# Kernel tuning notes

Hardware: AMD Instinct MI355X
Metric: run time of the kernel (lower is better)

The kernel has to match this reference:

```python
import jax, jax.numpy as jnp
import numpy as np

NUM_HEADS = 4
LN_EPS = 1e-5


def _gcn_layer(src, dst, feats, skip_w, skip_b, msg_w, msg_b):
    # DGL GCNLayer: symmetric degree norm (from src rows), copy_u+sum aggregation,
    # msg linear + affine skip. No activation is applied in the original forward.
    n = feats.shape[0]
    deg = jax.ops.segment_sum(jnp.ones(src.shape, feats.dtype), src, num_segments=n)
    dinv = jnp.where(deg > 0, deg ** -0.5, jnp.zeros_like(deg))
    h = feats * dinv[:, None]                                  # [N, D]
    agg = jax.ops.segment_sum(h[src], dst, num_segments=n)     # scatter-sum over edges
    rst = agg * dinv[:, None]
    return rst @ msg_w.T + msg_b + feats @ skip_w.T + skip_b


def _layernorm(x, g, b):
    mu = jnp.mean(x, axis=-1, keepdims=True)
    var = jnp.mean((x - mu) ** 2, axis=-1, keepdims=True)
    return (x - mu) * jax.lax.rsqrt(var + LN_EPS) * g + b


def _cross_attention(x, seq, in_proj_w, in_proj_b, out_proj_w, out_proj_b, ln_g, ln_b):
    # Unbatched torch nn.MultiheadAttention(query=x [N,D], key=value=seq [S,D]).
    n, d = x.shape
    hd = d // NUM_HEADS
    wq, wk, wv = in_proj_w[:d], in_proj_w[d:2 * d], in_proj_w[2 * d:]
    bq, bk, bv = in_proj_b[:d], in_proj_b[d:2 * d], in_proj_b[2 * d:]
    q = (x @ wq.T + bq).reshape(n, NUM_HEADS, hd)
    k = (seq @ wk.T + bk).reshape(-1, NUM_HEADS, hd)
    v = (seq @ wv.T + bv).reshape(-1, NUM_HEADS, hd)
    scores = jnp.einsum('nhd,shd->hns', q, k) / jnp.sqrt(jnp.asarray(hd, x.dtype))
    attn = jax.nn.softmax(scores, axis=-1)
    o = jnp.einsum('hns,shd->nhd', attn, v).reshape(n, d)
    o = o @ out_proj_w.T + out_proj_b
    # dropout is identity in eval mode; residual + layernorm (num_cross_att == 1 path)
    return _layernorm(o + x, ln_g, ln_b)


def reference(x, seq_embeddings, src, dst, edge_label_index,
              skip_w0, skip_b0, msg_w0, msg_b0,
              skip_w1, skip_b1, msg_w1, msg_b1,
              in_proj_w, in_proj_b, out_proj_w, out_proj_b, ln_g, ln_b,
              weight1, weight2):
    x = _gcn_layer(src, dst, x, skip_w0, skip_b0, msg_w0, msg_b0)
    x = _gcn_layer(src, dst, x, skip_w1, skip_b1, msg_w1, msg_b1)
    x = _cross_attention(x, seq_embeddings, in_proj_w, in_proj_b,
                         out_proj_w, out_proj_b, ln_g, ln_b)
    # F.normalize: row-wise L2
    x = x / jnp.maximum(jnp.linalg.norm(x, axis=-1, keepdims=True), 1e-12)
    node_embedding = x
    p = jax.nn.relu(x @ weight1.T)                # dropout identity (eval)
    p = jax.nn.sigmoid(p @ weight2.T)[:, 0]       # [N]
    # dot edge decoding over last dim of size 1 -> elementwise product
    pred = p[edge_label_index[0]] * p[edge_label_index[1]]
    return pred, node_embedding


def setup_inputs() -> dict:
    key = jax.random.key(0)
    ks = jax.random.split(key, 20)
    N, E, S, D, K = 8192, 524288, 2048, 128, 100000
    s = 1.0 / np.sqrt(D)  # xavier-ish scale for weight matrices
    inp = {
        'x': jax.random.normal(ks[0], (N, D), jnp.float32),
        'seq_embeddings': jax.random.normal(ks[1], (S, D), jnp.float32),
        'src': jax.random.randint(ks[2], (E,), 0, N, jnp.int32),
        'dst': jax.random.randint(ks[3], (E,), 0, N, jnp.int32),
        'edge_label_index': jax.random.randint(ks[4], (2, K), 0, N, jnp.int32),
        'skip_w0': jax.random.normal(ks[5], (D, D), jnp.float32) * s,
        'skip_b0': jnp.zeros((D,), jnp.float32),
        'msg_w0': jax.random.normal(ks[6], (D, D), jnp.float32) * s,
        'msg_b0': jnp.zeros((D,), jnp.float32),
        'skip_w1': jax.random.normal(ks[7], (D, D), jnp.float32) * s,
        'skip_b1': jnp.zeros((D,), jnp.float32),
        'msg_w1': jax.random.normal(ks[8], (D, D), jnp.float32) * s,
        'msg_b1': jnp.zeros((D,), jnp.float32),
        'in_proj_w': jax.random.normal(ks[9], (3 * D, D), jnp.float32) * s,
        'in_proj_b': jnp.zeros((3 * D,), jnp.float32),
        'out_proj_w': jax.random.normal(ks[10], (D, D), jnp.float32) * s,
        'out_proj_b': jnp.zeros((D,), jnp.float32),
        'ln_g': jnp.ones((D,), jnp.float32),
        'ln_b': jnp.zeros((D,), jnp.float32),
        'weight1': jax.random.normal(ks[11], (D, D), jnp.float32) * s,
        'weight2': jax.random.normal(ks[12], (1, D), jnp.float32) * s,
    }
    return inp
```

## Files before the change

kernel.cpp:

```cpp
#include <hip/hip_runtime.h>
#include <math.h>

#define D 128
#define HB 128
#define FA_PS 88

typedef short bf16x4 __attribute__((ext_vector_type(4)));
typedef short bf16x8 __attribute__((ext_vector_type(8)));
typedef float f32x4 __attribute__((ext_vector_type(4)));

__device__ __forceinline__ float4 ld4(const float* p) { return *(const float4*)p; }

__device__ __forceinline__ short f2bf_r(float f) {
  return (short)((__float_as_uint(f) + 0x8000u) >> 16);
}
__device__ __forceinline__ float bf2f(short s) {
  return __uint_as_float(((unsigned)(unsigned short)s) << 16);
}
__device__ __forceinline__ unsigned pack_bf2(float a, float b) {
  unsigned ua = __float_as_uint(a) + 0x8000u;
  unsigned ub = __float_as_uint(b) + 0x8000u;
  return __builtin_amdgcn_perm(ub, ua, 0x07060302);
}

struct WSrc { const float* p[9]; };
__global__ __launch_bounds__(256) void prep0_kernel(WSrc ws, short* __restrict__ Wbf,
                                                    const float* __restrict__ x,
                                                    short* __restrict__ xbf) {
  int b = blockIdx.x, t = threadIdx.x;
  if (b < 144) {
    int m = b >> 4, blk = b & 15;
    int i = (blk * 256 + t) * 4;
    float4 v = ld4(ws.p[m] + i);
    bf16x4 o = {f2bf_r(v.x), f2bf_r(v.y), f2bf_r(v.z), f2bf_r(v.w)};
    *(bf16x4*)&Wbf[m * 16384 + i] = o;
  } else {
    int i = ((b - 144) * 256 + t) * 4;
    float4 v = ld4(x + i);
    bf16x4 o = {f2bf_r(v.x), f2bf_r(v.y), f2bf_r(v.z), f2bf_r(v.w)};
    *(bf16x4*)&xbf[i] = o;
  }
}

__global__ __launch_bounds__(256) void hist_kernel(
    const int* __restrict__ src, const int* __restrict__ dst,
    int* __restrict__ histd, int* __restrict__ hists, int E) {
  __shared__ int hd[8192];
  __shared__ int hs[8192];
  int t = threadIdx.x;
  for (int i = t; i < 8192; i += 256) { hd[i] = 0; hs[i] = 0; }
  __syncthreads();
  int per = E / HB;
  int b0 = blockIdx.x * per;
  for (int j = 0; j < per; j += 256) {
    int i = b0 + j + t;
    atomicAdd(&hd[dst[i]], 1);
    atomicAdd(&hs[src[i]], 1);
  }
  __syncthreads();
  for (int i = t; i < 8192; i += 256) {
    histd[blockIdx.x * 8192 + i] = hd[i];
    hists[blockIdx.x * 8192 + i] = hs[i];
  }
}

__global__ __launch_bounds__(256) void colsum_kernel(
    const int* __restrict__ histd, const int* __restrict__ hists,
    int* __restrict__ deg, float* __restrict__ dinv) {
  int v = blockIdx.x * 256 + threadIdx.x;
  int sd = 0, ss = 0;
  for (int b = 0; b < HB; ++b) { sd += histd[b * 8192 + v]; ss += hists[b * 8192 + v]; }
  deg[v] = sd;
  dinv[v] = ss > 0 ? rsqrtf((float)ss) : 0.f;
}

__global__ __launch_bounds__(1024) void scan8k_kernel(
    const int* __restrict__ deg, int* __restrict__ row_ptr, int N) {
  __shared__ int wtot[16];
  int t = threadIdx.x;
  int lane = t & 63, wv = t >> 6;
  int v0 = t * 8;
  int x[8]; int s = 0;
#pragma unroll
  for (int j = 0; j < 8; ++j) { x[j] = s; s += deg[v0 + j]; }
  int incl = s;
  for (int off = 1; off < 64; off <<= 1) {
    int y = __shfl_up(incl, off);
    if (lane >= off) incl += y;
  }
  if (lane == 63) wtot[wv] = incl;
  __syncthreads();
  if (t == 0) { int run = 0; for (int i = 0; i < 16; ++i) { int v = wtot[i]; wtot[i] = run; run += v; } }
  __syncthreads();
  int base = wtot[wv] + (incl - s);
#pragma unroll
  for (int j = 0; j < 8; ++j) row_ptr[v0 + j] = base + x[j];
  if (t == 1023) row_ptr[N] = base + s;
}

__global__ __launch_bounds__(256) void basegen_kernel(
    const int* __restrict__ histd, const int* __restrict__ row_ptr,
    int* __restrict__ base_arr) {
  int v = blockIdx.x * 256 + threadIdx.x;
  int run = row_ptr[v];
  for (int b = 0; b < HB; ++b) { base_arr[b * 8192 + v] = run; run += histd[b * 8192 + v]; }
}

__global__ __launch_bounds__(256) void scatter2_kernel(
    const int* __restrict__ src, const int* __restrict__ dst,
    const int* __restrict__ base_arr, int* __restrict__ csr_src, int E) {
  __shared__ int lh[8192];
  int t = threadIdx.x;
  for (int i = t; i < 8192; i += 256) lh[i] = 0;
  __syncthreads();
  int per = E / HB;
  int b0 = blockIdx.x * per;
  const int* __restrict__ bb = &base_arr[blockIdx.x * 8192];
  for (int j = 0; j < per; j += 256) {
    int i = b0 + j + t;
    int v = dst[i];
    int r = atomicAdd(&lh[v], 1);
    csr_src[bb[v] + r] = src[i];
  }
}

__global__ __launch_bounds__(128) void agg_kernel(
    const short* __restrict__ fbf, const float* __restrict__ dinv,
    const int* __restrict__ row_ptr, const int* __restrict__ csr_src,
    short* __restrict__ outbf) {
  __shared__ int idx[128];
  __shared__ float dv[128];
  __shared__ float red[8][128];
  int n = blockIdx.x, t = threadIdx.x;
  int grp = t >> 4, l16 = t & 15;
  int beg = row_ptr[n], end = row_ptr[n + 1];
  float a0[8] = {}, a1[8] = {};
  for (int c = beg; c < end; c += 128) {
    int j = c + t;
    if (j < end) { int s = csr_src[j]; idx[t] = s; dv[t] = dinv[s]; }
    __syncthreads();
    int cnt = min(128, end - c);
    int e = grp;
    for (; e + 8 < cnt; e += 16) {
      bf16x8 w0 = *(const bf16x8*)&fbf[(size_t)idx[e] * D + l16 * 8];
      bf16x8 w1 = *(const bf16x8*)&fbf[(size_t)idx[e + 8] * D + l16 * 8];
      float wt0 = dv[e], wt1 = dv[e + 8];
#pragma unroll
      for (int k = 0; k < 8; ++k) {
        a0[k] += bf2f(w0[k]) * wt0;
        a1[k] += bf2f(w1[k]) * wt1;
      }
    }
    for (; e < cnt; e += 8) {
      bf16x8 w0 = *(const bf16x8*)&fbf[(size_t)idx[e] * D + l16 * 8];
      float wt0 = dv[e];
#pragma unroll
      for (int k = 0; k < 8; ++k) a0[k] += bf2f(w0[k]) * wt0;
    }
    __syncthreads();
  }
#pragma unroll
  for (int k = 0; k < 8; ++k) a0[k] += a1[k];
  *(float4*)&red[grp][l16 * 8] = *(float4*)&a0[0];
  *(float4*)&red[grp][l16 * 8 + 4] = *(float4*)&a0[4];
  __syncthreads();
  if (t < 32) {
    int d0 = t * 4;
    float o[4] = {};
#pragma unroll
    for (int g = 0; g < 8; ++g) {
      o[0] += red[g][d0]; o[1] += red[g][d0 + 1];
      o[2] += red[g][d0 + 2]; o[3] += red[g][d0 + 3];
    }
    float w = dinv[n];
    bf16x4 ov = {f2bf_r(o[0] * w), f2bf_r(o[1] * w), f2bf_r(o[2] * w), f2bf_r(o[3] * w)};
    *(bf16x4*)&outbf[(size_t)n * D + d0] = ov;
  }
}

__device__ __forceinline__ void mfma_accum(const short* As, const short* __restrict__ W,
                                           int rt, int ch, int quad, int r16, f32x4* acc) {
#pragma unroll
  for (int ks = 0; ks < 4; ++ks) {
    bf16x8 af = *(bf16x8*)&As[(rt * 16 + r16) * 136 + ks * 32 + quad * 8];
#pragma unroll
    for (int nt = 0; nt < 4; ++nt) {
      bf16x8 bw = *(const bf16x8*)&W[(size_t)(ch * 64 + nt * 16 + r16) * D + ks * 32 + quad * 8];
      acc[nt] = __builtin_amdgcn_mfma_f32_16x16x32_bf16(af, bw, acc[nt], 0, 0, 0);
    }
  }
}

__device__ __forceinline__ void stage_A_f32(const float* __restrict__ A, int m0, short* As) {
  int row = threadIdx.x >> 3, seg = threadIdx.x & 7;
  const float* ap = &A[(size_t)(m0 + row) * D + seg * 16];
  float4 v0 = ld4(ap), v1 = ld4(ap + 4), v2 = ld4(ap + 8), v3 = ld4(ap + 12);
  bf16x8 w0 = {f2bf_r(v0.x), f2bf_r(v0.y), f2bf_r(v0.z), f2bf_r(v0.w),
               f2bf_r(v1.x), f2bf_r(v1.y), f2bf_r(v1.z), f2bf_r(v1.w)};
  bf16x8 w1 = {f2bf_r(v2.x), f2bf_r(v2.y), f2bf_r(v2.z), f2bf_r(v2.w),
               f2bf_r(v3.x), f2bf_r(v3.y), f2bf_r(v3.z), f2bf_r(v3.w)};
  *(bf16x8*)&As[row * 136 + seg * 16] = w0;
  *(bf16x8*)&As[row * 136 + seg * 16 + 8] = w1;
}

__device__ __forceinline__ void stage_A_bf16(const short* __restrict__ A, int m0, short* As) {
  int row = threadIdx.x >> 3, seg = threadIdx.x & 7;
  const short* ap = &A[(size_t)(m0 + row) * D + seg * 16];
  bf16x8 a0 = *(const bf16x8*)ap;
  bf16x8 a1 = *(const bf16x8*)(ap + 8);
  *(bf16x8*)&As[row * 136 + seg * 16] = a0;
  *(bf16x8*)&As[row * 136 + seg * 16 + 8] = a1;
}

__global__ __launch_bounds__(256) void gemm_gcn_kernel(
    const short* __restrict__ A1, const short* __restrict__ W1, const float* __restrict__ b1,
    const short* __restrict__ A2, const short* __restrict__ W2, const float* __restrict__ b2,
    short* __restrict__ Cbf, float* __restrict__ Cf) {
  __shared__ short As[32 * 136];
  const int t = threadIdx.x;
  const int m0 = blockIdx.x * 32;
  const int w = t >> 6, lane = t & 63, quad = lane >> 4, r16 = lane & 15;
  const int rt = w & 1, ch = w >> 1;
  f32x4 acc[4];
  f32x4 zz = {0.f, 0.f, 0.f, 0.f};
  acc[0] = zz; acc[1] = zz; acc[2] = zz; acc[3] = zz;
  stage_A_bf16(A1, m0, As);
  __syncthreads();
  mfma_accum(As, W1, rt, ch, quad, r16, acc);
  __syncthreads();
  stage_A_bf16(A2, m0, As);
  __syncthreads();
  mfma_accum(As, W2, rt, ch, quad, r16, acc);
#pragma unroll
  for (int nt = 0; nt < 4; ++nt) {
    int col = ch * 64 + nt * 16 + r16;
    float bias = b1[col] + b2[col];
#pragma unroll
    for (int g = 0; g < 4; ++g) {
      int row = m0 + rt * 16 + quad * 4 + g;
      float v = acc[nt][g] + bias;
      if (Cbf) Cbf[(size_t)row * D + col] = f2bf_r(v);
      if (Cf) Cf[(size_t)row * D + col] = v;
    }
  }
}

__global__ __launch_bounds__(256) void qkv_kernel(
    const float* __restrict__ B2, const float* __restrict__ seq,
    const short* __restrict__ Wq, const short* __restrict__ Wk, const short* __restrict__ Wv,
    const float* __restrict__ ipb,
    short* __restrict__ Qbf, float* __restrict__ qn,
    short* __restrict__ Kbf, int* __restrict__ MkhI,
    short* __restrict__ Vt, int N, int S) {
  __shared__ short As[32 * 136];
  __shared__ int lmax[4];
  const int t = threadIdx.x;
  const int b = blockIdx.x;
  const int w = t >> 6, lane = t & 63, quad = lane >> 4, r16 = lane & 15;
  const int rt = w & 1, ch = w >> 1;
  if (t < 4) lmax[t] = 0;
  f32x4 acc[4];
  f32x4 zz = {0.f, 0.f, 0.f, 0.f};
  acc[0] = zz; acc[1] = zz; acc[2] = zz; acc[3] = zz;
  const float SC = 0.25503473f;

  if (b < 256) {
    int m0 = b * 32;
    stage_A_f32(B2, m0, As);
    __syncthreads();
    mfma_accum(As, Wq, rt, ch, quad, r16, acc);
    float pq[4][2] = {};
#pragma unroll
    for (int nt = 0; nt < 4; ++nt) {
      int col = ch * 64 + nt * 16 + r16;
      float bias = ipb[col];
      int p = nt >> 1;
#pragma unroll
      for (int g = 0; g < 4; ++g) {
        int row = m0 + rt * 16 + quad * 4 + g;
        float vs = (acc[nt][g] + bias) * SC;
        Qbf[(size_t)row * D + col] = f2bf_r(vs);
        pq[g][p] += vs * vs;
      }
    }
#pragma unroll
    for (int mask = 1; mask < 16; mask <<= 1)
#pragma unroll
      for (int g = 0; g < 4; ++g) {
        pq[g][0] += __shfl_xor(pq[g][0], mask);
        pq[g][1] += __shfl_xor(pq[g][1], mask);
      }
    if (r16 == 0) {
#pragma unroll
      for (int g = 0; g < 4; ++g) {
        int row = m0 + rt * 16 + quad * 4 + g;
        qn[(ch * 2 + 0) * N + row] = sqrtf(pq[g][0]);
        qn[(ch * 2 + 1) * N + row] = sqrtf(pq[g][1]);
      }
    }
  } else if (b < 320) {
    int m0 = (b - 256) * 32;
    stage_A_f32(seq, m0, As);
    __syncthreads();
    mfma_accum(As, Wk, rt, ch, quad, r16, acc);
    float pk[4][2] = {};
#pragma unroll
    for (int nt = 0; nt < 4; ++nt) {
      int col = ch * 64 + nt * 16 + r16;
      float bias = ipb[128 + col];
      int p = nt >> 1;
#pragma unroll
      for (int g = 0; g < 4; ++g) {
        int key = m0 + rt * 16 + quad * 4 + g;
        float v = acc[nt][g] + bias;
        Kbf[(size_t)key * D + col] = f2bf_r(v);
        pk[g][p] += v * v;
      }
    }
#pragma unroll
    for (int mask = 1; mask < 16; mask <<= 1)
#pragma unroll
      for (int g = 0; g < 4; ++g) {
        pk[g][0] += __shfl_xor(pk[g][0], mask);
        pk[g][1] += __shfl_xor(pk[g][1], mask);
      }
    if (r16 == 0) {
#pragma unroll
      for (int g = 0; g < 4; ++g) {
        atomicMax(&lmax[ch * 2 + 0], __float_as_int(pk[g][0]));
        atomicMax(&lmax[ch * 2 + 1], __float_as_int(pk[g][1]));
      }
    }
    __syncthreads();
    if (t < 4) atomicMax(&MkhI[t], lmax[t]);
  } else {
    int m0 = (b - 320) * 32;
    stage_A_f32(seq, m0, As);
    __syncthreads();
    mfma_accum(As, Wv, rt, ch, quad, r16, acc);
#pragma unroll
    for (int nt = 0; nt < 4; ++nt) {
      int dim = ch * 64 + nt * 16 + r16;
      float bias = ipb[256 + dim];
#pragma unroll
      for (int g = 0; g < 4; ++g) {
        int s = m0 + rt * 16 + quad * 4 + g;
        int local = s & 63;
        int kp = (local & 15) * 4 + (local >> 4);
        int gcol = (s & ~63) + kp;
        Vt[(size_t)dim * S + gcol] = f2bf_r(acc[nt][g] + bias);
      }
    }
  }
}

__global__ __launch_bounds__(64, 4) void flash_kernel(
    const short* __restrict__ Qbf, const short* __restrict__ Kbf, const short* __restrict__ Vt,
    const float* __restrict__ qn, const int* __restrict__ MkhI,
    float* __restrict__ Osp, float* __restrict__ lbuf, int N, int S) {
  __shared__ short Ps[32 * FA_PS];
  const int lane = threadIdx.x;
  const int quad = lane >> 4, r16 = lane & 15;
  const int n0 = blockIdx.x * 32;
  const int h = blockIdx.y;
  const int sp = blockIdx.z;
  float* O = Osp + (size_t)sp * N * D;

  bf16x8 aq[2];
  aq[0] = *(const bf16x8*)&Qbf[(size_t)(n0 + r16) * D + h * 32 + quad * 8];
  aq[1] = *(const bf16x8*)&Qbf[(size_t)(n0 + 16 + r16) * D + h * 32 + quad * 8];

  float sqm = sqrtf(fmaxf(__int_as_float(MkhI[h]), 0.f));
  float msh[2][4];
#pragma unroll
  for (int rt = 0; rt < 2; ++rt)
#pragma unroll
    for (int g = 0; g < 4; ++g)
      msh[rt][g] = fminf(qn[h * N + n0 + rt * 16 + quad * 4 + g] * sqm, 57.7f);

  f32x4 o[2][2], lac[2];
  f32x4 zz = {0.f, 0.f, 0.f, 0.f};
  o[0][0] = zz; o[0][1] = zz; o[1][0] = zz; o[1][1] = zz;
  lac[0] = zz; lac[1] = zz;
  bf16x8 ones = {(short)0x3F80, (short)0x3F80, (short)0x3F80, (short)0x3F80,
                 (short)0x3F80, (short)0x3F80, (short)0x3F80, (short)0x3F80};

  const int span = S >> 2;
  const int c0 = sp * span;
  for (int c = c0; c < c0 + span; c += 64) {
    f32x4 s[2][4];
#pragma unroll
    for (int kt = 0; kt < 4; ++kt) {
      bf16x8 bk = *(const bf16x8*)&Kbf[(size_t)(c + kt * 16 + r16) * D + h * 32 + quad * 8];
      f32x4 z = {0.f, 0.f, 0.f, 0.f};
      s[0][kt] = __builtin_amdgcn_mfma_f32_16x16x32_bf16(aq[0], bk, z, 0, 0, 0);
      s[1][kt] = __builtin_amdgcn_mfma_f32_16x16x32_bf16(aq[1], bk, z, 0, 0, 0);
    }
#pragma unroll
    for (int rt = 0; rt < 2; ++rt)
#pragma unroll
      for (int g = 0; g < 4; ++g) {
        float m = msh[rt][g];
        float p0 = exp2f(s[rt][0][g] - m);
        float p1 = exp2f(s[rt][1][g] - m);
        float p2 = exp2f(s[rt][2][g] - m);
        float p3 = exp2f(s[rt][3][g] - m);
        uint2 uv = {pack_bf2(p0, p1), pack_bf2(p2, p3)};
        *(uint2*)&Ps[(rt * 16 + quad * 4 + g) * FA_PS + r16 * 4] = uv;
      }
    bf16x8 bv[2][2];
#pragma unroll
    for (int kc = 0; kc < 2; ++kc)
#pragma unroll
      for (int nt = 0; nt < 2; ++nt)
        bv[kc][nt] = *(const bf16x8*)&Vt[(size_t)(h * 32 + nt * 16 + r16) * S + c + kc * 32 + quad * 8];
#pragma unroll
    for (int rt = 0; rt < 2; ++rt)
#pragma unroll
      for (int kc = 0; kc < 2; ++kc) {
        bf16x8 ap = *(bf16x8*)&Ps[(rt * 16 + r16) * FA_PS + kc * 32 + quad * 8];
        lac[rt] = __builtin_amdgcn_mfma_f32_16x16x32_bf16(ap, ones, lac[rt], 0, 0, 0);
#pragma unroll
        for (int nt = 0; nt < 2; ++nt)
          o[rt][nt] = __builtin_amdgcn_mfma_f32_16x16x32_bf16(ap, bv[kc][nt], o[rt][nt], 0, 0, 0);
      }
  }
#pragma unroll
  for (int rt = 0; rt < 2; ++rt)
#pragma unroll
    for (int g = 0; g < 4; ++g) {
      int row = n0 + rt * 16 + quad * 4 + g;
#pragma unroll
      for (int nt = 0; nt < 2; ++nt)
        O[(size_t)row * D + h * 32 + nt * 16 + r16] = o[rt][nt][g];
      if (r16 == 0) lbuf[(sp * 4 + h) * N + row] = lac[rt][g];
    }
}

__global__ __launch_bounds__(256) void gemm_op_kernel(
    const float* __restrict__ Osp, const float* __restrict__ lbuf,
    const short* __restrict__ W, const float* __restrict__ bias,
    const float* __restrict__ Rres, const float* __restrict__ ln_g,
    const float* __restrict__ ln_b, float* __restrict__ emb, int N) {
  __shared__ short As[32 * 136];
  __shared__ float Cs[32 * 132];
  const int t = threadIdx.x;
  const int m0 = blockIdx.x * 32;
  const int w = t >> 6, lane = t & 63, quad = lane >> 4, r16 = lane & 15;
  const int rt = w & 1, ch = w >> 1;
  {
    int row = t >> 3, seg = t & 7;
    int grow = m0 + row;
    int hh = seg >> 1;
    float l = lbuf[hh * N + grow] + lbuf[(4 + hh) * N + grow] +
              lbuf[(8 + hh) * N + grow] + lbuf[(12 + hh) * N + grow];
    float inv = 1.f / l;
    const float* p = &Osp[(size_t)grow * D + seg * 16];
    size_t st = (size_t)N * D;
    float a16[16];
#pragma unroll
    for (int q = 0; q < 4; ++q) {
      float4 a = ld4(p + q * 4), b = ld4(p + st + q * 4),
             c = ld4(p + 2 * st + q * 4), d = ld4(p + 3 * st + q * 4);
      a16[q * 4 + 0] = (a.x + b.x + c.x + d.x) * inv;
      a16[q * 4 + 1] = (a.y + b.y + c.y + d.y) * inv;
      a16[q * 4 + 2] = (a.z + b.z + c.z + d.z) * inv;
      a16[q * 4 + 3] = (a.w + b.w + c.w + d.w) * inv;
    }
    bf16x8 w0 = {f2bf_r(a16[0]), f2bf_r(a16[1]), f2bf_r(a16[2]), f2bf_r(a16[3]),
                 f2bf_r(a16[4]), f2bf_r(a16[5]), f2bf_r(a16[6]), f2bf_r(a16[7])};
    bf16x8 w1 = {f2bf_r(a16[8]), f2bf_r(a16[9]), f2bf_r(a16[10]), f2bf_r(a16[11]),
                 f2bf_r(a16[12]), f2bf_r(a16[13]), f2bf_r(a16[14]), f2bf_r(a16[15])};
    *(bf16x8*)&As[row * 136 + seg * 16] = w0;
    *(bf16x8*)&As[row * 136 + seg * 16 + 8] = w1;
  }
  __syncthreads();
  f32x4 acc[4];
  f32x4 zz = {0.f, 0.f, 0.f, 0.f};
  acc[0] = zz; acc[1] = zz; acc[2] = zz; acc[3] = zz;
  mfma_accum(As, W, rt, ch, quad, r16, acc);
#pragma unroll
  for (int nt = 0; nt < 4; ++nt) {
    int col = ch * 64 + nt * 16 + r16;
    float bs = bias[col];
#pragma unroll
    for (int g = 0; g < 4; ++g) {
      int lr = rt * 16 + quad * 4 + g;
      Cs[lr * 132 + col] = acc[nt][g] + bs + Rres[(size_t)(m0 + lr) * D + col];
    }
  }
  __syncthreads();
  {
    int row = t >> 3, seg = t & 7;
    float xv[16];
#pragma unroll
    for (int q = 0; q < 4; ++q) {
      f32x4 v = *(f32x4*)&Cs[row * 132 + seg * 16 + q * 4];
      xv[q * 4] = v[0]; xv[q * 4 + 1] = v[1]; xv[q * 4 + 2] = v[2]; xv[q * 4 + 3] = v[3];
    }
    float s = 0.f, sq = 0.f;
#pragma unroll
    for (int k = 0; k < 16; ++k) { s += xv[k]; sq += xv[k] * xv[k]; }
#pragma unroll
    for (int mask = 1; mask < 8; mask <<= 1) { s += __shfl_xor(s, mask); sq += __shfl_xor(sq, mask); }
    float mu = s * (1.f / 128.f);
    float var = fmaxf(sq * (1.f / 128.f) - mu * mu, 0.f);
    float rs = rsqrtf(var + 1e-5f);
    float yv[16], nn = 0.f;
#pragma unroll
    for (int q = 0; q < 4; ++q) {
      float4 gg = ld4(&ln_g[seg * 16 + q * 4]);
      float4 bb = ld4(&ln_b[seg * 16 + q * 4]);
      float y0 = (xv[q * 4] - mu) * rs * gg.x + bb.x;
      float y1 = (xv[q * 4 + 1] - mu) * rs * gg.y + bb.y;
      float y2 = (xv[q * 4 + 2] - mu) * rs * gg.z + bb.z;
      float y3 = (xv[q * 4 + 3] - mu) * rs * gg.w + bb.w;
      yv[q * 4] = y0; yv[q * 4 + 1] = y1; yv[q * 4 + 2] = y2; yv[q * 4 + 3] = y3;
      nn += y0 * y0 + y1 * y1 + y2 * y2 + y3 * y3;
    }
#pragma unroll
    for (int mask = 1; mask < 8; mask <<= 1) nn += __shfl_xor(nn, mask);
    float inv = 1.f / fmaxf(sqrtf(nn), 1e-12f);
#pragma unroll
    for (int q = 0; q < 4; ++q) {
      float4 ov = {yv[q * 4] * inv, yv[q * 4 + 1] * inv, yv[q * 4 + 2] * inv, yv[q * 4 + 3] * inv};
      *(float4*)&emb[(size_t)(m0 + row) * D + seg * 16 + q * 4] = ov;
    }
  }
}

__global__ __launch_bounds__(256) void gemm_mlp_kernel(
    const float* __restrict__ emb, const short* __restrict__ W,
    const float* __restrict__ w2, float* __restrict__ pbuf) {
  __shared__ short As[32 * 136];
  __shared__ float part[32][2];
  const int t = threadIdx.x;
  const int m0 = blockIdx.x * 32;
  const int w = t >> 6, lane = t & 63, quad = lane >> 4, r16 = lane & 15;
  const int rt = w & 1, ch = w >> 1;
  stage_A_f32(emb, m0, As);
  __syncthreads();
  f32x4 acc[4];
  f32x4 zz = {0.f, 0.f, 0.f, 0.f};
  acc[0] = zz; acc[1] = zz; acc[2] = zz; acc[3] = zz;
  mfma_accum(As, W, rt, ch, quad, r16, acc);
  float pg[4] = {};
#pragma unroll
  for (int nt = 0; nt < 4; ++nt) {
    float wv = w2[ch * 64 + nt * 16 + r16];
#pragma unroll
    for (int g = 0; g < 4; ++g) pg[g] += fmaxf(acc[nt][g], 0.f) * wv;
  }
#pragma unroll
  for (int mask = 1; mask < 16; mask <<= 1)
#pragma unroll
    for (int g = 0; g < 4; ++g) pg[g] += __shfl_xor(pg[g], mask);
  if (r16 == 0) {
#pragma unroll
    for (int g = 0; g < 4; ++g) part[rt * 16 + quad * 4 + g][ch] = pg[g];
  }
  __syncthreads();
  if (t < 32) {
    float sv = part[t][0] + part[t][1];
    pbuf[m0 + t] = 1.f / (1.f + __expf(-sv));
  }
}

__global__ void pred_kernel(const float* __restrict__ p, const int* __restrict__ eli,
                            float* __restrict__ out, int K) {
  int i = blockIdx.x * blockDim.x + threadIdx.x;
  if (i < K) out[i] = p[eli[i]] * p[eli[K + i]];
}

extern "C" void kernel_launch(void* const* d_in, const int* in_sizes, int n_in,
                              void* d_out, int out_size, void* d_ws, size_t ws_size,
                              hipStream_t stream) {
  const float* x       = (const float*)d_in[0];
  const float* seq     = (const float*)d_in[1];
  const int* src       = (const int*)d_in[2];
  const int* dst       = (const int*)d_in[3];
  const int* eli       = (const int*)d_in[4];
  const float* skip_w0 = (const float*)d_in[5];
  const float* skip_b0 = (const float*)d_in[6];
  const float* msg_w0  = (const float*)d_in[7];
  const float* msg_b0  = (const float*)d_in[8];
  const float* skip_w1 = (const float*)d_in[9];
  const float* skip_b1 = (const float*)d_in[10];
  const float* msg_w1  = (const float*)d_in[11];
  const float* msg_b1  = (const float*)d_in[12];
  const float* ipw     = (const float*)d_in[13];
  const float* ipb     = (const float*)d_in[14];
  const float* opw     = (const float*)d_in[15];
  const float* opb     = (const float*)d_in[16];
  const float* ln_g    = (const float*)d_in[17];
  const float* ln_b    = (const float*)d_in[18];
  const float* w1      = (const float*)d_in[19];
  const float* w2      = (const float*)d_in[20];

  const int N  = in_sizes[0] / D;
  const int S  = in_sizes[1] / D;
  const int E  = in_sizes[2];
  const int Kp = in_sizes[4] / 2;

  float* ws    = (float*)d_ws;
  float* B2    = ws;
  float* Osp   = B2 + (size_t)N * D;
  short* xbf   = (short*)(Osp + 4 * (size_t)N * D);
  short* Abf   = xbf + (size_t)N * D;
  short* B1bf  = Abf + (size_t)N * D;
  short* Qbf   = B1bf + (size_t)N * D;
  short* Kbf   = Qbf + (size_t)N * D;
  short* Vt    = Kbf + (size_t)S * D;
  short* Wbf   = Vt + (size_t)D * S;
  float* qn    = (float*)(Wbf + 9 * 16384);
  float* lbuf  = qn + 4 * (size_t)N;
  float* dinv  = lbuf + 16 * (size_t)N;
  float* pbuf  = dinv + N;
  int*   MkhI  = (int*)(pbuf + N);
  int* deg     = MkhI + 4;
  int* row_ptr = deg + N;
  int* csr_src = row_ptr + (N + 1);
  int* histd   = csr_src + E;
  int* hists   = histd + HB * 8192;
  int* base_arr= hists + HB * 8192;

  float* pred_out = (float*)d_out;
  float* emb_out  = pred_out + Kp;

  const short* w_skip0 = Wbf + 0 * 16384;
  const short* w_msg0  = Wbf + 1 * 16384;
  const short* w_skip1 = Wbf + 2 * 16384;
  const short* w_msg1  = Wbf + 3 * 16384;
  const short* w_q     = Wbf + 4 * 16384;
  const short* w_k     = Wbf + 5 * 16384;
  const short* w_v     = Wbf + 6 * 16384;
  const short* w_op    = Wbf + 7 * 16384;
  const short* w_m1    = Wbf + 8 * 16384;

  hipMemsetAsync(MkhI, 0, 4 * sizeof(int), stream);

  WSrc wsrc;
  wsrc.p[0] = skip_w0; wsrc.p[1] = msg_w0; wsrc.p[2] = skip_w1; wsrc.p[3] = msg_w1;
  wsrc.p[4] = ipw; wsrc.p[5] = ipw + D * D; wsrc.p[6] = ipw + 2 * D * D;
  wsrc.p[7] = opw; wsrc.p[8] = w1;
  prep0_kernel<<<144 + (N * D / 1024), 256, 0, stream>>>(wsrc, (short*)Wbf, x, xbf);

  hist_kernel<<<HB, 256, 0, stream>>>(src, dst, histd, hists, E);
  colsum_kernel<<<N / 256, 256, 0, stream>>>(histd, hists, deg, dinv);
  scan8k_kernel<<<1, 1024, 0, stream>>>(deg, row_ptr, N);
  basegen_kernel<<<N / 256, 256, 0, stream>>>(histd, row_ptr, base_arr);
  scatter2_kernel<<<HB, 256, 0, stream>>>(src, dst, base_arr, csr_src, E);

  agg_kernel<<<N, 128, 0, stream>>>(xbf, dinv, row_ptr, csr_src, Abf);
  gemm_gcn_kernel<<<N / 32, 256, 0, stream>>>(Abf, w_msg0, msg_b0, xbf, w_skip0, skip_b0, B1bf, nullptr);
  agg_kernel<<<N, 128, 0, stream>>>(B1bf, dinv, row_ptr, csr_src, Abf);
  gemm_gcn_kernel<<<N / 32, 256, 0, stream>>>(Abf, w_msg1, msg_b1, B1bf, w_skip1, skip_b1, nullptr, B2);

  qkv_kernel<<<N / 32 + 2 * (S / 32), 256, 0, stream>>>(
      B2, seq, w_q, w_k, w_v, ipb, Qbf, qn, Kbf, MkhI, Vt, N, S);

  dim3 fgrid(N / 32, 4, 4);
  flash_kernel<<<fgrid, 64, 0, stream>>>(Qbf, Kbf, Vt, qn, MkhI, Osp, lbuf, N, S);
  gemm_op_kernel<<<N / 32, 256, 0, stream>>>(Osp, lbuf, w_op, opb, B2, ln_g, ln_b, emb_out, N);

  gemm_mlp_kernel<<<N / 32, 256, 0, stream>>>(emb_out, w_m1, w2, pbuf);
  pred_kernel<<<(Kp + 255) / 256, 256, 0, stream>>>(pbuf, eli, pred_out, Kp);
}
```

Measured before the change: 238.4 us.

## Fuse CSR build into one grid-synced kernel, widen flash splits and agg unroll

```diff
diff --git a/kernel.cpp b/kernel.cpp
--- a/kernel.cpp
+++ b/kernel.cpp
@@ -4,6 +4,7 @@
 #define D 128
 #define HB 128
 #define FA_PS 88
+#define SPLITS 8
 
 typedef short bf16x4 __attribute__((ext_vector_type(4)));
 typedef short bf16x8 __attribute__((ext_vector_type(8)));
@@ -23,11 +24,29 @@
   return __builtin_amdgcn_perm(ub, ua, 0x07060302);
 }
 
+__device__ __forceinline__ void gsync(int* bar, int target) {
+  __syncthreads();
+  __threadfence();
+  if (threadIdx.x == 0) {
+    __hip_atomic_fetch_add(bar, 1, __ATOMIC_RELEASE, __HIP_MEMORY_SCOPE_AGENT);
+    while (__hip_atomic_load(bar, __ATOMIC_ACQUIRE, __HIP_MEMORY_SCOPE_AGENT) < target)
+      __builtin_amdgcn_s_sleep(4);
+  }
+  __syncthreads();
+  __threadfence();
+}
+
 struct WSrc { const float* p[9]; };
 __global__ __launch_bounds__(256) void prep0_kernel(WSrc ws, short* __restrict__ Wbf,
                                                     const float* __restrict__ x,
-                                                    short* __restrict__ xbf) {
+                                                    short* __restrict__ xbf,
+                                                    int* __restrict__ bar,
+                                                    int* __restrict__ MkhI) {
   int b = blockIdx.x, t = threadIdx.x;
+  if (b == 0 && t == 0) {
+    *bar = 0;
+    MkhI[0] = 0; MkhI[1] = 0; MkhI[2] = 0; MkhI[3] = 0;
+  }
   if (b < 144) {
     int m = b >> 4, blk = b & 15;
     int i = (blk * 256 + t) * 4;
@@ -42,16 +61,20 @@
   }
 }
 
-__global__ __launch_bounds__(256) void hist_kernel(
+__global__ __launch_bounds__(256) void csr_kernel(
     const int* __restrict__ src, const int* __restrict__ dst,
-    int* __restrict__ histd, int* __restrict__ hists, int E) {
+    int* __restrict__ histd, int* __restrict__ hists,
+    int* __restrict__ base_arr, int* __restrict__ csr_src,
+    float* __restrict__ dinv, int* __restrict__ row_ptr,
+    int* __restrict__ bsum, int* bar, int E, int N) {
   __shared__ int hd[8192];
   __shared__ int hs[8192];
-  int t = threadIdx.x;
+  const int t = threadIdx.x;
+  const int b = blockIdx.x;
+  const int per = E / HB;
+  const int b0 = b * per;
   for (int i = t; i < 8192; i += 256) { hd[i] = 0; hs[i] = 0; }
   __syncthreads();
-  int per = E / HB;
-  int b0 = blockIdx.x * per;
   for (int j = 0; j < per; j += 256) {
     int i = b0 + j + t;
     atomicAdd(&hd[dst[i]], 1);
@@ -59,68 +82,48 @@
   }
   __syncthreads();
   for (int i = t; i < 8192; i += 256) {
-    histd[blockIdx.x * 8192 + i] = hd[i];
-    hists[blockIdx.x * 8192 + i] = hs[i];
-  }
-}
-
-__global__ __launch_bounds__(256) void colsum_kernel(
-    const int* __restrict__ histd, const int* __restrict__ hists,
-    int* __restrict__ deg, float* __restrict__ dinv) {
-  int v = blockIdx.x * 256 + threadIdx.x;
-  int sd = 0, ss = 0;
-  for (int b = 0; b < HB; ++b) { sd += histd[b * 8192 + v]; ss += hists[b * 8192 + v]; }
-  deg[v] = sd;
-  dinv[v] = ss > 0 ? rsqrtf((float)ss) : 0.f;
-}
-
-__global__ __launch_bounds__(1024) void scan8k_kernel(
-    const int* __restrict__ deg, int* __restrict__ row_ptr, int N) {
-  __shared__ int wtot[16];
-  int t = threadIdx.x;
-  int lane = t & 63, wv = t >> 6;
-  int v0 = t * 8;
-  int x[8]; int s = 0;
-#pragma unroll
-  for (int j = 0; j < 8; ++j) { x[j] = s; s += deg[v0 + j]; }
-  int incl = s;
-  for (int off = 1; off < 64; off <<= 1) {
-    int y = __shfl_up(incl, off);
-    if (lane >= off) incl += y;
-  }
-  if (lane == 63) wtot[wv] = incl;
-  __syncthreads();
-  if (t == 0) { int run = 0; for (int i = 0; i < 16; ++i) { int v = wtot[i]; wtot[i] = run; run += v; } }
-  __syncthreads();
-  int base = wtot[wv] + (incl - s);
-#pragma unroll
-  for (int j = 0; j < 8; ++j) row_ptr[v0 + j] = base + x[j];
-  if (t == 1023) row_ptr[N] = base + s;
-}
-
-__global__ __launch_bounds__(256) void basegen_kernel(
-    const int* __restrict__ histd, const int* __restrict__ row_ptr,
-    int* __restrict__ base_arr) {
-  int v = blockIdx.x * 256 + threadIdx.x;
-  int run = row_ptr[v];
-  for (int b = 0; b < HB; ++b) { base_arr[b * 8192 + v] = run; run += histd[b * 8192 + v]; }
-}
-
-__global__ __launch_bounds__(256) void scatter2_kernel(
-    const int* __restrict__ src, const int* __restrict__ dst,
-    const int* __restrict__ base_arr, int* __restrict__ csr_src, int E) {
-  __shared__ int lh[8192];
-  int t = threadIdx.x;
-  for (int i = t; i < 8192; i += 256) lh[i] = 0;
-  __syncthreads();
-  int per = E / HB;
-  int b0 = blockIdx.x * per;
-  const int* __restrict__ bb = &base_arr[blockIdx.x * 8192];
+    histd[b * 8192 + i] = hd[i];
+    hists[b * 8192 + i] = hs[i];
+  }
+  int sd = 0;
+  int v = b * 64 + (t & 63);
+  gsync(bar, HB);
+  if (t < 64) {
+    int ss = 0;
+    for (int k = 0; k < HB; ++k) { sd += histd[k * 8192 + v]; ss += hists[k * 8192 + v]; }
+    dinv[v] = ss > 0 ? rsqrtf((float)ss) : 0.f;
+    int tot = sd;
+#pragma unroll
+    for (int off = 32; off; off >>= 1) tot += __shfl_xor(tot, off);
+    if (t == 0) bsum[b] = tot;
+  }
+  gsync(bar, 2 * HB);
+  if (t < 64) {
+    int x = (t < b) ? bsum[t] : 0;
+    if (t + 64 < b) x += bsum[t + 64];
+#pragma unroll
+    for (int off = 32; off; off >>= 1) x += __shfl_xor(x, off);
+    int incl = sd;
+#pragma unroll
+    for (int off = 1; off < 64; off <<= 1) {
+      int y = __shfl_up(incl, off);
+      if ((t & 63) >= off) incl += y;
+    }
+    int base = x + incl - sd;
+    row_ptr[v] = base;
+    if (b == HB - 1 && t == 63) row_ptr[N] = x + incl;
+    int run = base;
+    for (int k = 0; k < HB; ++k) { base_arr[k * 8192 + v] = run; run += histd[k * 8192 + v]; }
+  }
+  gsync(bar, 3 * HB);
+  for (int i = t; i < 8192; i += 256) hd[i] = 0;
+  __syncthreads();
+  const int* __restrict__ bb = &base_arr[b * 8192];
   for (int j = 0; j < per; j += 256) {
     int i = b0 + j + t;
-    int v = dst[i];
-    int r = atomicAdd(&lh[v], 1);
-    csr_src[bb[v] + r] = src[i];
+    int vv = dst[i];
+    int r = atomicAdd(&hd[vv], 1);
+    csr_src[bb[vv] + r] = src[i];
   }
 }
 
@@ -134,21 +137,25 @@
   int n = blockIdx.x, t = threadIdx.x;
   int grp = t >> 4, l16 = t & 15;
   int beg = row_ptr[n], end = row_ptr[n + 1];
-  float a0[8] = {}, a1[8] = {};
+  float a0[8] = {}, a1[8] = {}, a2[8] = {}, a3[8] = {};
   for (int c = beg; c < end; c += 128) {
     int j = c + t;
     if (j < end) { int s = csr_src[j]; idx[t] = s; dv[t] = dinv[s]; }
     __syncthreads();
     int cnt = min(128, end - c);
     int e = grp;
-    for (; e + 8 < cnt; e += 16) {
+    for (; e + 24 < cnt; e += 32) {
       bf16x8 w0 = *(const bf16x8*)&fbf[(size_t)idx[e] * D + l16 * 8];
       bf16x8 w1 = *(const bf16x8*)&fbf[(size_t)idx[e + 8] * D + l16 * 8];
-      float wt0 = dv[e], wt1 = dv[e + 8];
+      bf16x8 w2 = *(const bf16x8*)&fbf[(size_t)idx[e + 16] * D + l16 * 8];
+      bf16x8 w3 = *(const bf16x8*)&fbf[(size_t)idx[e + 24] * D + l16 * 8];
+      float wt0 = dv[e], wt1 = dv[e + 8], wt2 = dv[e + 16], wt3 = dv[e + 24];
 #pragma unroll
       for (int k = 0; k < 8; ++k) {
         a0[k] += bf2f(w0[k]) * wt0;
         a1[k] += bf2f(w1[k]) * wt1;
+        a2[k] += bf2f(w2[k]) * wt2;
+        a3[k] += bf2f(w3[k]) * wt3;
       }
     }
     for (; e < cnt; e += 8) {
@@ -160,7 +167,7 @@
     __syncthreads();
   }
 #pragma unroll
-  for (int k = 0; k < 8; ++k) a0[k] += a1[k];
+  for (int k = 0; k < 8; ++k) a0[k] += a1[k] + a2[k] + a3[k];
   *(float4*)&red[grp][l16 * 8] = *(float4*)&a0[0];
   *(float4*)&red[grp][l16 * 8 + 4] = *(float4*)&a0[4];
   __syncthreads();
@@ -354,7 +361,7 @@
   }
 }
 
-__global__ __launch_bounds__(64, 4) void flash_kernel(
+__global__ __launch_bounds__(64, 8) void flash_kernel(
     const short* __restrict__ Qbf, const short* __restrict__ Kbf, const short* __restrict__ Vt,
     const float* __restrict__ qn, const int* __restrict__ MkhI,
     float* __restrict__ Osp, float* __restrict__ lbuf, int N, int S) {
@@ -385,7 +392,7 @@
   bf16x8 ones = {(short)0x3F80, (short)0x3F80, (short)0x3F80, (short)0x3F80,
                  (short)0x3F80, (short)0x3F80, (short)0x3F80, (short)0x3F80};
 
-  const int span = S >> 2;
+  const int span = S / SPLITS;
   const int c0 = sp * span;
   for (int c = c0; c < c0 + span; c += 64) {
     f32x4 s[2][4];
@@ -452,21 +459,24 @@
     int row = t >> 3, seg = t & 7;
     int grow = m0 + row;
     int hh = seg >> 1;
-    float l = lbuf[hh * N + grow] + lbuf[(4 + hh) * N + grow] +
-              lbuf[(8 + hh) * N + grow] + lbuf[(12 + hh) * N + grow];
+    float l = 0.f;
+#pragma unroll
+    for (int s = 0; s < SPLITS; ++s) l += lbuf[(s * 4 + hh) * N + grow];
     float inv = 1.f / l;
     const float* p = &Osp[(size_t)grow * D + seg * 16];
     size_t st = (size_t)N * D;
-    float a16[16];
-#pragma unroll
-    for (int q = 0; q < 4; ++q) {
-      float4 a = ld4(p + q * 4), b = ld4(p + st + q * 4),
-             c = ld4(p + 2 * st + q * 4), d = ld4(p + 3 * st + q * 4);
-      a16[q * 4 + 0] = (a.x + b.x + c.x + d.x) * inv;
-      a16[q * 4 + 1] = (a.y + b.y + c.y + d.y) * inv;
-      a16[q * 4 + 2] = (a.z + b.z + c.z + d.z) * inv;
-      a16[q * 4 + 3] = (a.w + b.w + c.w + d.w) * inv;
-    }
+    float a16[16] = {};
+#pragma unroll
+    for (int s = 0; s < SPLITS; ++s) {
+#pragma unroll
+      for (int q = 0; q < 4; ++q) {
+        float4 a = ld4(p + s * st + q * 4);
+        a16[q * 4 + 0] += a.x; a16[q * 4 + 1] += a.y;
+        a16[q * 4 + 2] += a.z; a16[q * 4 + 3] += a.w;
+      }
+    }
+#pragma unroll
+    for (int k = 0; k < 16; ++k) a16[k] *= inv;
     bf16x8 w0 = {f2bf_r(a16[0]), f2bf_r(a16[1]), f2bf_r(a16[2]), f2bf_r(a16[3]),
                  f2bf_r(a16[4]), f2bf_r(a16[5]), f2bf_r(a16[6]), f2bf_r(a16[7])};
     bf16x8 w1 = {f2bf_r(a16[8]), f2bf_r(a16[9]), f2bf_r(a16[10]), f2bf_r(a16[11]),
@@ -605,7 +615,7 @@
   float* ws    = (float*)d_ws;
   float* B2    = ws;
   float* Osp   = B2 + (size_t)N * D;
-  short* xbf   = (short*)(Osp + 4 * (size_t)N * D);
+  short* xbf   = (short*)(Osp + (size_t)SPLITS * N * D);
   short* Abf   = xbf + (size_t)N * D;
   short* B1bf  = Abf + (size_t)N * D;
   short* Qbf   = B1bf + (size_t)N * D;
@@ -614,11 +624,12 @@
   short* Wbf   = Vt + (size_t)D * S;
   float* qn    = (float*)(Wbf + 9 * 16384);
   float* lbuf  = qn + 4 * (size_t)N;
-  float* dinv  = lbuf + 16 * (size_t)N;
+  float* dinv  = lbuf + 4 * (size_t)SPLITS * N;
   float* pbuf  = dinv + N;
   int*   MkhI  = (int*)(pbuf + N);
-  int* deg     = MkhI + 4;
-  int* row_ptr = deg + N;
+  int*   bar   = MkhI + 4;
+  int*   bsum  = bar + 1;
+  int* row_ptr = bsum + HB;
   int* csr_src = row_ptr + (N + 1);
   int* histd   = csr_src + E;
   int* hists   = histd + HB * 8192;
@@ -637,19 +648,14 @@
   const short* w_op    = Wbf + 7 * 16384;
   const short* w_m1    = Wbf + 8 * 16384;
 
-  hipMemsetAsync(MkhI, 0, 4 * sizeof(int), stream);
-
   WSrc wsrc;
   wsrc.p[0] = skip_w0; wsrc.p[1] = msg_w0; wsrc.p[2] = skip_w1; wsrc.p[3] = msg_w1;
   wsrc.p[4] = ipw; wsrc.p[5] = ipw + D * D; wsrc.p[6] = ipw + 2 * D * D;
   wsrc.p[7] = opw; wsrc.p[8] = w1;
-  prep0_kernel<<<144 + (N * D / 1024), 256, 0, stream>>>(wsrc, (short*)Wbf, x, xbf);
-
-  hist_kernel<<<HB, 256, 0, stream>>>(src, dst, histd, hists, E);
-  colsum_kernel<<<N / 256, 256, 0, stream>>>(histd, hists, deg, dinv);
-  scan8k_kernel<<<1, 1024, 0, stream>>>(deg, row_ptr, N);
-  basegen_kernel<<<N / 256, 256, 0, stream>>>(histd, row_ptr, base_arr);
-  scatter2_kernel<<<HB, 256, 0, stream>>>(src, dst, base_arr, csr_src, E);
+  prep0_kernel<<<144 + (N * D / 1024), 256, 0, stream>>>(wsrc, (short*)Wbf, x, xbf, bar, MkhI);
+
+  csr_kernel<<<HB, 256, 0, stream>>>(src, dst, histd, hists, base_arr, csr_src,
+                                     dinv, row_ptr, bsum, bar, E, N);
 
   agg_kernel<<<N, 128, 0, stream>>>(xbf, dinv, row_ptr, csr_src, Abf);
   gemm_gcn_kernel<<<N / 32, 256, 0, stream>>>(Abf, w_msg0, msg_b0, xbf, w_skip0, skip_b0, B1bf, nullptr);
@@ -659,7 +665,7 @@
   qkv_kernel<<<N / 32 + 2 * (S / 32), 256, 0, stream>>>(
       B2, seq, w_q, w_k, w_v, ipb, Qbf, qn, Kbf, MkhI, Vt, N, S);
 
-  dim3 fgrid(N / 32, 4, 4);
+  dim3 fgrid(N / 32, 4, SPLITS);
   flash_kernel<<<fgrid, 64, 0, stream>>>(Qbf, Kbf, Vt, qn, MkhI, Osp, lbuf, N, S);
   gemm_op_kernel<<<N / 32, 256, 0, stream>>>(Osp, lbuf, w_op, opb, B2, ln_g, ln_b, emb_out, N);
 
```

New measurement: 357.1 us. +49.8%, slower.
